# Optimization experiments

Measured on AMD Instinct MI355X. Metric: run time of the kernel, lower is better.

The kernel has to match this reference:

```python
import jax, jax.numpy as jnp
import numpy as np

LONG, LAT, T, B, H, NL = 64, 64, 12, 1024, 256, 2
N = LONG * LAT        # 4096 grid nodes
D = 16 * 16           # 256, lin1_size**2


def _build_adj():
    # Faithful reconstruction of GNNLayer's sparse COO adjacency (duplicates sum,
    # as torch sparse matmul does): identity + symmetric 8-neighbor stencil for
    # interior indices i in [lat+1, (long-1)*lat-1). Each undirected edge is
    # inserted twice (once from each endpoint's loop), so interior weights are 2.
    A = np.zeros((N, N), np.float32)
    A[np.arange(N), np.arange(N)] = 1.0
    i = np.arange(LAT + 1, (LONG - 1) * LAT - 1)
    offs = np.array([-1, 1, LAT, -LAT, LAT - 1, LAT + 1, -LAT - 1, -LAT + 1])
    rows = np.repeat(i, 8)
    cols = (i[:, None] + offs).ravel()
    np.add.at(A, (rows, cols), 1.0)
    np.add.at(A, (cols, rows), 1.0)
    return jnp.asarray(A)


def setup_inputs() -> dict:
    key = jax.random.key(0)
    ks = jax.random.split(key, 12)
    s = lambda k, shape, fan: (jax.random.normal(k, shape, jnp.float32) / np.sqrt(fan)).astype(jnp.float32)
    return {
        "x":  jax.random.normal(ks[0], (T, B, LONG, LAT), jnp.float32),
        "h0": jax.random.normal(ks[1], (NL, B, H), jnp.float32),
        "A":  _build_adj(),
        "W_gnn": s(ks[2], (D, N), N), "b_gnn": jnp.zeros((D,), jnp.float32),
        "W_lin": s(ks[3], (D, D), D), "b_lin": jnp.zeros((D,), jnp.float32),
        "Wih0": s(ks[4], (3 * H, D), D), "Whh0": s(ks[5], (3 * H, H), H),
        "bih0": jnp.zeros((3 * H,), jnp.float32), "bhh0": jnp.zeros((3 * H,), jnp.float32),
        "Wih1": s(ks[6], (3 * H, H), H), "Whh1": s(ks[7], (3 * H, H), H),
        "bih1": jnp.zeros((3 * H,), jnp.float32), "bhh1": jnp.zeros((3 * H,), jnp.float32),
        "Wf0": s(ks[8], (16, H), H), "bf0": jnp.zeros((16,), jnp.float32),
        "Wf1": s(ks[9], (16, 16), 16), "bf1": jnp.zeros((16,), jnp.float32),
        "Wf2": s(ks[10], (1, 16), 16), "bf2": jnp.zeros((1,), jnp.float32),
    }


def _gru_layer(xs, h0, Wih, Whh, bih, bhh):
    # xs: [T, B, In]; PyTorch GRU cell equations, input projection hoisted out of scan.
    xW = jnp.einsum('tbd,hd->tbh', xs, Wih) + bih  # [T, B, 3H]
    def step(h, xw):
        hW = h @ Whh.T + bhh
        ri, zi, ni = jnp.split(xw, 3, axis=-1)
        rh, zh, nh = jnp.split(hW, 3, axis=-1)
        r = jax.nn.sigmoid(ri + rh)
        z = jax.nn.sigmoid(zi + zh)
        n = jnp.tanh(ni + r * nh)
        hn = (1.0 - z) * n + z * h
        return hn, hn
    _, hs = jax.lax.scan(step, h0, xW)
    return hs  # [T, B, H]


def reference(x, h0, A, W_gnn, b_gnn, W_lin, b_lin,
              Wih0, Whh0, bih0, bhh0, Wih1, Whh1, bih1, bhh1,
              Wf0, bf0, Wf1, bf1, Wf2, bf2):
    xf = x.reshape(T, B, N)                                   # flatten grid per step
    h1 = jnp.einsum('tbn,mn->tbm', xf, A)                     # (A @ x^T)^T, all steps at once
    t2 = jax.nn.sigmoid(h1 @ W_gnn.T + b_gnn)                 # GNNLayer lin1 + sigmoid
    t4 = jax.nn.sigmoid(t2 @ W_lin.T + b_lin)                 # HailNet lin1 + sigmoid -> [T,B,256]
    hs = _gru_layer(t4, h0[0], Wih0, Whh0, bih0, bhh0)
    hs = _gru_layer(hs, h0[1], Wih1, Whh1, bih1, bhh1)
    out = hs[-1]                                              # last timestep, [B, H]
    out = jax.nn.sigmoid(out @ Wf0.T + bf0)
    out = jax.nn.sigmoid(out @ Wf1.T + bf1)
    out = jax.nn.sigmoid(out @ Wf2.T + bf2)                   # [B, 1]
    return out
```

## Files before the change

### kernel.cpp

```cpp
#include <hip/hip_runtime.h>
#include <hip/hip_bf16.h>

typedef __bf16 bf16;
typedef __bf16 bf16x4 __attribute__((ext_vector_type(4)));
typedef __bf16 bf16x8 __attribute__((ext_vector_type(8)));
typedef float  f32x4  __attribute__((ext_vector_type(4)));

__device__ __forceinline__ float sigf(float x) { return 1.f / (1.f + __expf(-x)); }
__device__ __forceinline__ float tanhf_fast(float x) { return 1.f - 2.f / (1.f + __expf(2.f * x)); }


__global__ __launch_bounds__(256) void k_weff(const float* __restrict__ A,
                                              const float* __restrict__ Wg,
                                              bf16* __restrict__ Weff) {
    int n = blockIdx.x * 256 + threadIdx.x;
    const int offs[9] = {0, -1, 1, 64, -64, 63, 65, -65, -63};
    float w[9];
    int   m[9];
#pragma unroll
    for (int j = 0; j < 9; j++) {
        int mm = n + offs[j];
        bool ok = (mm >= 0 && mm < 4096);
        m[j] = ok ? mm : 0;
        w[j] = ok ? A[(size_t)n * 4096 + mm] : 0.f;
    }
    int d0 = blockIdx.y * 8;
    for (int d = d0; d < d0 + 8; d++) {
        const float* wr = Wg + (size_t)d * 4096;
        float acc = 0.f;
#pragma unroll
        for (int j = 0; j < 9; j++) acc += w[j] * wr[m[j]];
        Weff[(size_t)d * 4096 + n] = (bf16)acc;
    }
}

__device__ __forceinline__ void prep_conv(const float* __restrict__ a,
                                          bf16* __restrict__ o, int blk) {
    int i = blk * 256 + threadIdx.x;
    o[i] = (bf16)a[i];
}

__device__ __forceinline__ void prep_pack(const float* __restrict__ W,
                                          bf16* __restrict__ out, int blk) {
    int fl = blk * 256 + threadIdx.x;
    int lane = fl & 63;
    int kt = (fl >> 6) & 7;
    int c  = (fl >> 9) % 6;
    int wv = (fl >> 9) / 6;
    int l16 = lane & 15, q = lane >> 4;
    int g = c >> 1;
    int wr = g * 256 + wv * 32 + (c & 1) * 16 + l16;
    const float* p = W + (size_t)wr * 256 + kt * 32 + q * 8;
    float4 f0 = *(const float4*)p, f1 = *(const float4*)(p + 4);
    bf16x8 v;
    v[0] = (bf16)f0.x; v[1] = (bf16)f0.y; v[2] = (bf16)f0.z; v[3] = (bf16)f0.w;
    v[4] = (bf16)f1.x; v[5] = (bf16)f1.y; v[6] = (bf16)f1.z; v[7] = (bf16)f1.w;
    *(bf16x8*)(out + (size_t)fl * 8) = v;
}

__global__ __launch_bounds__(256) void k_prep(const float* __restrict__ Wlin, bf16* __restrict__ WlinB,
                                              const float* __restrict__ Wih0, bf16* __restrict__ Wih0B,
                                              const float* __restrict__ Wih1, bf16* __restrict__ Wih1B,
                                              const float* __restrict__ Whh0, bf16* __restrict__ Wpk0,
                                              const float* __restrict__ Whh1, bf16* __restrict__ Wpk1) {
    int b = blockIdx.x;
    if (b < 256)        prep_conv(Wlin, WlinB, b);
    else if (b < 1024)  prep_conv(Wih0, Wih0B, b - 256);
    else if (b < 1792)  prep_conv(Wih1, Wih1B, b - 1024);
    else if (b < 1888)  prep_pack(Whh0, Wpk0, b - 1792);
    else                prep_pack(Whh1, Wpk1, b - 1888);
}

template <int K, int NTOT, int ACT, bool AF32>
__global__ __launch_bounds__(256) void k_gemm(const void* __restrict__ Ap,
                                              const bf16* __restrict__ Bp,
                                              const float* __restrict__ bias,
                                              void* __restrict__ Cp) {
    __shared__ bf16 sA[64 * 40];
    __shared__ bf16 sB[256 * 40];
    const int tid = threadIdx.x;
    const int lane = tid & 63, wv = tid >> 6;
    const int l16 = lane & 15, q = lane >> 4;
    const int row0 = blockIdx.x * 64;
    const int col0 = blockIdx.y * 256;
    const int ar = tid >> 2, ak = (tid & 3) * 8;

    f32x4 acc[4][4] = {};
    float4 pa0, pa1;
    bf16x8 pab;
    bf16x8 pb[4];

    auto loadA = [&](int k0) {
        if (AF32) {
            const float* p = (const float*)Ap + (size_t)(row0 + ar) * K + k0 + ak;
            pa0 = *(const float4*)p;
            pa1 = *(const float4*)(p + 4);
        } else {
            const bf16* p = (const bf16*)Ap + (size_t)(row0 + ar) * K + k0 + ak;
            pab = *(const bf16x8*)p;
        }
    };
    auto loadB = [&](int k0) {
#pragma unroll
        for (int i = 0; i < 4; i++) {
            int idx = tid + i * 256;
            int r = idx >> 2, kk = (idx & 3) * 8;
            pb[i] = *(const bf16x8*)(Bp + (size_t)(col0 + r) * K + k0 + kk);
        }
    };
    auto stage = [&]() {
        if (AF32) {
            bf16x8 v;
            v[0] = (bf16)pa0.x; v[1] = (bf16)pa0.y; v[2] = (bf16)pa0.z; v[3] = (bf16)pa0.w;
            v[4] = (bf16)pa1.x; v[5] = (bf16)pa1.y; v[6] = (bf16)pa1.z; v[7] = (bf16)pa1.w;
            *(bf16x8*)(sA + ar * 40 + ak) = v;
        } else {
            *(bf16x8*)(sA + ar * 40 + ak) = pab;
        }
#pragma unroll
        for (int i = 0; i < 4; i++) {
            int idx = tid + i * 256;
            int r = idx >> 2, kk = (idx & 3) * 8;
            *(bf16x8*)(sB + r * 40 + kk) = pb[i];
        }
    };

    loadA(0);
    loadB(0);
    const int S = K / 32;
    for (int s = 0; s < S; s++) {
        stage();
        __syncthreads();
        if (s + 1 < S) { loadA((s + 1) * 32); loadB((s + 1) * 32); }
        bf16x8 af[4], bfr[4];
#pragma unroll
        for (int tm = 0; tm < 4; tm++)
            af[tm] = *(bf16x8*)(sA + (tm * 16 + l16) * 40 + q * 8);
#pragma unroll
        for (int tn = 0; tn < 4; tn++)
            bfr[tn] = *(bf16x8*)(sB + (wv * 64 + tn * 16 + l16) * 40 + q * 8);
#pragma unroll
        for (int tm = 0; tm < 4; tm++)
#pragma unroll
            for (int tn = 0; tn < 4; tn++)
                acc[tm][tn] = __builtin_amdgcn_mfma_f32_16x16x32_bf16(
                    af[tm], bfr[tn], acc[tm][tn], 0, 0, 0);
        __syncthreads();
    }

#pragma unroll
    for (int tm = 0; tm < 4; tm++)
#pragma unroll
        for (int tn = 0; tn < 4; tn++)
#pragma unroll
            for (int r = 0; r < 4; r++) {
                int row = row0 + tm * 16 + q * 4 + r;
                int col = col0 + wv * 64 + tn * 16 + l16;
                float v = acc[tm][tn][r] + bias[col];
                if (ACT == 1)
                    ((bf16*)Cp)[(size_t)row * NTOT + col] = (bf16)sigf(v);
                else
                    ((float*)Cp)[(size_t)row * NTOT + col] = v;
            }
}

template <int K, int CHUNK>
__global__ __launch_bounds__(256) void k_gemm_sk(const float* __restrict__ Ap,
                                                 const bf16* __restrict__ Bp,
                                                 float* __restrict__ Cpart) {
    __shared__ bf16 sA[64 * 40];
    __shared__ bf16 sB[256 * 40];
    const int tid = threadIdx.x;
    const int lane = tid & 63, wv = tid >> 6;
    const int l16 = lane & 15, q = lane >> 4;
    const int row0 = blockIdx.x * 64;
    const int kb = blockIdx.y * CHUNK;
    float* Cp = Cpart + (size_t)blockIdx.y * 12288 * 256;
    const int ar = tid >> 2, ak = (tid & 3) * 8;

    f32x4 acc[4][4] = {};
    float4 pa0, pa1;
    bf16x8 pb[4];

    auto loadA = [&](int k0) {
        const float* p = Ap + (size_t)(row0 + ar) * K + kb + k0 + ak;
        pa0 = *(const float4*)p;
        pa1 = *(const float4*)(p + 4);
    };
    auto loadB = [&](int k0) {
#pragma unroll
        for (int i = 0; i < 4; i++) {
            int idx = tid + i * 256;
            int r = idx >> 2, kk = (idx & 3) * 8;
            pb[i] = *(const bf16x8*)(Bp + (size_t)r * K + kb + k0 + kk);
        }
    };
    auto stage = [&]() {
        bf16x8 v;
        v[0] = (bf16)pa0.x; v[1] = (bf16)pa0.y; v[2] = (bf16)pa0.z; v[3] = (bf16)pa0.w;
        v[4] = (bf16)pa1.x; v[5] = (bf16)pa1.y; v[6] = (bf16)pa1.z; v[7] = (bf16)pa1.w;
        *(bf16x8*)(sA + ar * 40 + ak) = v;
#pragma unroll
        for (int i = 0; i < 4; i++) {
            int idx = tid + i * 256;
            int r = idx >> 2, kk = (idx & 3) * 8;
            *(bf16x8*)(sB + r * 40 + kk) = pb[i];
        }
    };

    loadA(0);
    loadB(0);
    const int S = CHUNK / 32;
    for (int s = 0; s < S; s++) {
        stage();
        __syncthreads();
        if (s + 1 < S) { loadA((s + 1) * 32); loadB((s + 1) * 32); }
        bf16x8 af[4], bfr[4];
#pragma unroll
        for (int tm = 0; tm < 4; tm++)
            af[tm] = *(bf16x8*)(sA + (tm * 16 + l16) * 40 + q * 8);
#pragma unroll
        for (int tn = 0; tn < 4; tn++)
            bfr[tn] = *(bf16x8*)(sB + (wv * 64 + tn * 16 + l16) * 40 + q * 8);
#pragma unroll
        for (int tm = 0; tm < 4; tm++)
#pragma unroll
            for (int tn = 0; tn < 4; tn++)
                acc[tm][tn] = __builtin_amdgcn_mfma_f32_16x16x32_bf16(
                    af[tm], bfr[tn], acc[tm][tn], 0, 0, 0);
        __syncthreads();
    }

#pragma unroll
    for (int tm = 0; tm < 4; tm++)
#pragma unroll
        for (int tn = 0; tn < 4; tn++)
#pragma unroll
            for (int r = 0; r < 4; r++) {
                int row = row0 + tm * 16 + q * 4 + r;
                int col = wv * 64 + tn * 16 + l16;
                Cp[(size_t)row * 256 + col] = acc[tm][tn][r];
            }
}

template <int KS>
__global__ __launch_bounds__(256) void k_reduce(const float* __restrict__ Cpart,
                                                const float* __restrict__ bias,
                                                bf16* __restrict__ t2) {
    const size_t STRIDE = (size_t)12288 * 256;
    size_t i = ((size_t)blockIdx.x * 256 + threadIdx.x) * 4;
    f32x4 s = *(const f32x4*)(Cpart + i);
#pragma unroll
    for (int ks = 1; ks < KS; ks++) {
        f32x4 p = *(const f32x4*)(Cpart + ks * STRIDE + i);
        s[0] += p[0]; s[1] += p[1]; s[2] += p[2]; s[3] += p[3];
    }
    int col = (int)(i & 255);
    const float4 b = *(const float4*)(bias + col);
    bf16x4 o;
    o[0] = (bf16)sigf(s[0] + b.x);
    o[1] = (bf16)sigf(s[1] + b.y);
    o[2] = (bf16)sigf(s[2] + b.z);
    o[3] = (bf16)sigf(s[3] + b.w);
    *(bf16x4*)(t2 + i) = o;
}

__global__ __launch_bounds__(512, 2) void k_gru(const float* __restrict__ xw,
                                                const bf16* __restrict__ Wpk,
                                                const float* __restrict__ bhh,
                                                const float* __restrict__ h0,
                                                bf16* __restrict__ hs_out,
                                                float* __restrict__ hfin) {
    __shared__ bf16 hl[16 * 264];
    __shared__ float xwl[16 * 772];
    const int tid = threadIdx.x, lane = tid & 63, wv = tid >> 6;
    const int l16 = lane & 15, q = lane >> 4;
    const int row0 = blockIdx.x * 16;
    const bf16* wb = Wpk + (size_t)wv * 6 * 8 * 64 * 8;

    float bh[6];
#pragma unroll
    for (int c = 0; c < 6; c++) {
        int g = c >> 1;
        bh[c] = bhh[g * 256 + wv * 32 + (c & 1) * 16 + l16];
    }
    float hreg[2][4];
#pragma unroll
    for (int hc = 0; hc < 2; hc++)
#pragma unroll
        for (int r = 0; r < 4; r++) {
            int row = q * 4 + r, col = wv * 32 + hc * 16 + l16;
            float h = h0[(size_t)(row0 + row) * 256 + col];
            hreg[hc][r] = h;
            hl[row * 264 + col] = (bf16)h;
        }
    __syncthreads();

    for (int t = 0; t < 12; t++) {
        {
            const float* gbase = xw + ((size_t)t * 1024 + row0) * 768;
#pragma unroll
            for (int rr = 0; rr < 2; rr++) {
                int row = wv * 2 + rr;
#pragma unroll
                for (int i = 0; i < 3; i++) {
                    const float* gp = gbase + (size_t)row * 768 + i * 256 + lane * 4;
                    float* lp = xwl + row * 772 + i * 256;
                    __builtin_amdgcn_global_load_lds(
                        (const __attribute__((address_space(1))) void*)gp,
                        (__attribute__((address_space(3))) void*)lp,
                        16, 0, 0);
                }
            }
        }
        f32x4 acc[6] = {};
        bf16x8 bc[6], bn[6];
#pragma unroll
        for (int c = 0; c < 6; c++)
            bc[c] = *(const bf16x8*)(wb + ((size_t)(c * 8 + 0) * 64 + lane) * 8);
#pragma unroll
        for (int kt = 0; kt < 8; kt++) {
            bf16x8 a = *(bf16x8*)(hl + l16 * 264 + kt * 32 + q * 8);
            if (kt < 7) {
#pragma unroll
                for (int c = 0; c < 6; c++)
                    bn[c] = *(const bf16x8*)(wb + ((size_t)(c * 8 + kt + 1) * 64 + lane) * 8);
            }
#pragma unroll
            for (int c = 0; c < 6; c++)
                acc[c] = __builtin_amdgcn_mfma_f32_16x16x32_bf16(a, bc[c], acc[c], 0, 0, 0);
#pragma unroll
            for (int c = 0; c < 6; c++) bc[c] = bn[c];
        }
        __syncthreads();
#pragma unroll
        for (int hc = 0; hc < 2; hc++)
#pragma unroll
            for (int r = 0; r < 4; r++) {
                int row = q * 4 + r, col = wv * 32 + hc * 16 + l16;
                const float* xb = xwl + row * 772 + col;
                float rv = sigf(xb[0] + acc[hc][r] + bh[hc]);
                float zv = sigf(xb[256] + acc[2 + hc][r] + bh[2 + hc]);
                float nv = tanhf_fast(xb[512] + rv * (acc[4 + hc][r] + bh[4 + hc]));
                float hn = (1.f - zv) * nv + zv * hreg[hc][r];
                hreg[hc][r] = hn;
                bf16 hb = (bf16)hn;
                hl[row * 264 + col] = hb;
                if (hs_out) hs_out[((size_t)t * 1024 + row0 + row) * 256 + col] = hb;
            }
        __syncthreads();
    }
    if (hfin) {
#pragma unroll
        for (int hc = 0; hc < 2; hc++)
#pragma unroll
            for (int r = 0; r < 4; r++) {
                int row = q * 4 + r, col = wv * 32 + hc * 16 + l16;
                hfin[(size_t)(row0 + row) * 256 + col] = hreg[hc][r];
            }
    }
}

__global__ __launch_bounds__(256) void k_final(const float* __restrict__ h,
                                               const float* __restrict__ Wf0, const float* __restrict__ bf0,
                                               const float* __restrict__ Wf1, const float* __restrict__ bf1,
                                               const float* __restrict__ Wf2, const float* __restrict__ bf2,
                                               float* __restrict__ out) {
    __shared__ float sh[16 * 257];
    __shared__ float sy0[16 * 17];
    __shared__ float sy1[16 * 17];
    int tid = threadIdx.x;
    int r0 = blockIdx.x * 16;
#pragma unroll
    for (int i = 0; i < 16; i++) {
        int idx = tid + i * 256;
        int rr = idx >> 8, cc = idx & 255;
        sh[rr * 257 + cc] = h[(size_t)(r0 + rr) * 256 + cc];
    }
    __syncthreads();
    int rl = tid >> 4, j = tid & 15;
    float acc = bf0[j];
    for (int k = 0; k < 256; k++) acc += sh[rl * 257 + k] * Wf0[j * 256 + k];
    sy0[rl * 17 + j] = sigf(acc);
    __syncthreads();
    float acc1 = bf1[j];
#pragma unroll
    for (int k = 0; k < 16; k++) acc1 += sy0[rl * 17 + k] * Wf1[j * 16 + k];
    sy1[rl * 17 + j] = sigf(acc1);
    __syncthreads();
    if (tid < 16) {
        float a2 = bf2[0];
#pragma unroll
        for (int k = 0; k < 16; k++) a2 += sy1[tid * 17 + k] * Wf2[k];
        out[r0 + tid] = sigf(a2);
    }
}

extern "C" void kernel_launch(void* const* d_in, const int* in_sizes, int n_in,
                              void* d_out, int out_size, void* d_ws, size_t ws_size,
                              hipStream_t stream) {
    const float* x    = (const float*)d_in[0];
    const float* h0   = (const float*)d_in[1];
    const float* A    = (const float*)d_in[2];
    const float* Wgnn = (const float*)d_in[3];
    const float* bgnn = (const float*)d_in[4];
    const float* Wlin = (const float*)d_in[5];
    const float* blin = (const float*)d_in[6];
    const float* Wih0 = (const float*)d_in[7];
    const float* Whh0 = (const float*)d_in[8];
    const float* bih0 = (const float*)d_in[9];
    const float* bhh0 = (const float*)d_in[10];
    const float* Wih1 = (const float*)d_in[11];
    const float* Whh1 = (const float*)d_in[12];
    const float* bih1 = (const float*)d_in[13];
    const float* bhh1 = (const float*)d_in[14];
    const float* Wf0  = (const float*)d_in[15];
    const float* bf0  = (const float*)d_in[16];
    const float* Wf1  = (const float*)d_in[17];
    const float* bf1  = (const float*)d_in[18];
    const float* Wf2  = (const float*)d_in[19];
    const float* bf2  = (const float*)d_in[20];
    float* out = (float*)d_out;

    char* w = (char*)d_ws;
    bf16* Weff  = (bf16*)w;  w += (size_t)256 * 4096 * 2;
    bf16* WlinB = (bf16*)w;  w += (size_t)256 * 256 * 2;
    bf16* Wih0B = (bf16*)w;  w += (size_t)768 * 256 * 2;
    bf16* Wih1B = (bf16*)w;  w += (size_t)768 * 256 * 2;
    bf16* Wpk0  = (bf16*)w;  w += (size_t)768 * 256 * 2;
    bf16* Wpk1  = (bf16*)w;  w += (size_t)768 * 256 * 2;
    bf16* t2    = (bf16*)w;  w += (size_t)12288 * 256 * 2;
    bf16* t4    = (bf16*)w;  w += (size_t)12288 * 256 * 2;
    float* Cpart = (float*)w;
    float* xwb  = (float*)w;
    bf16*  hs   = (bf16*)(w + (size_t)12288 * 768 * 4);
    float* hfin = (float*)(w + (size_t)12288 * 768 * 4 + (size_t)12288 * 256 * 2);
    w += (size_t)4 * 12288 * 256 * 4;
    (void)ws_size;

    k_weff<<<dim3(16, 32), 256, 0, stream>>>(A, Wgnn, Weff);
    k_prep<<<dim3(1984), 256, 0, stream>>>(Wlin, WlinB, Wih0, Wih0B, Wih1, Wih1B,
                                           Whh0, Wpk0, Whh1, Wpk1);

    k_gemm_sk<4096, 2048><<<dim3(192, 2), 256, 0, stream>>>(x, Weff, Cpart);
    k_reduce<2><<<dim3(3072), 256, 0, stream>>>(Cpart, bgnn, t2);
    k_gemm<256, 256, 1, false><<<dim3(192, 1), 256, 0, stream>>>(t2, WlinB, blin, t4);
    k_gemm<256, 768, 0, false><<<dim3(192, 3), 256, 0, stream>>>(t4, Wih0B, bih0, xwb);
    k_gru<<<dim3(64), 512, 0, stream>>>(xwb, Wpk0, bhh0, h0, hs, nullptr);
    k_gemm<256, 768, 0, false><<<dim3(192, 3), 256, 0, stream>>>(hs, Wih1B, bih1, xwb);
    k_gru<<<dim3(64), 512, 0, stream>>>(xwb, Wpk1, bhh1, h0 + (size_t)1024 * 256, nullptr, hfin);
    k_final<<<dim3(64), 256, 0, stream>>>(hfin, Wf0, bf0, Wf1, bf1, Wf2, bf2, out);
}
```

Before: 557.2 us.

## Replace split-K GEMM plus reduce with N-tiled full-K GEMM fused with sigmoid

The large x·Weff GEMM (K=4096) used a split-K scheme writing fp32 partials that a separate reduce kernel summed, biased and passed through a sigmoid. It is now one kernel that tiles N into 64-column blocks (grid 192x4) and runs the full K loop with a 64-wide K step, applying bias and sigmoid in the epilogue. This removes the partial-sum round trip through global memory and one launch. In exchange each x row tile is re-read and re-converted once per N block (four times), and each block does less MFMA work per shared-memory stage.

```diff
diff --git a/kernel.cpp b/kernel.cpp
--- a/kernel.cpp
+++ b/kernel.cpp
@@ -71,6 +71,75 @@
     else                prep_pack(Whh1, Wpk1, b - 1888);
 }
 
+__global__ __launch_bounds__(256) void k_gemm_x(const float* __restrict__ Ap,
+                                                const bf16* __restrict__ Bp,
+                                                const float* __restrict__ bias,
+                                                bf16* __restrict__ Cp) {
+    __shared__ bf16 sA[64 * 72];
+    __shared__ bf16 sB[64 * 72];
+    const int tid = threadIdx.x;
+    const int lane = tid & 63, wv = tid >> 6;
+    const int l16 = lane & 15, q = lane >> 4;
+    const int row0 = blockIdx.x * 64;
+    const int col0 = blockIdx.y * 64;
+    const int ar = tid >> 2, ak = (tid & 3) * 16;
+
+    f32x4 acc[4] = {};
+    float4 pa0, pa1, pa2, pa3;
+    bf16x8 pb0, pb1;
+
+    auto loadA = [&](int k0) {
+        const float* p = Ap + (size_t)(row0 + ar) * 4096 + k0 + ak;
+        pa0 = *(const float4*)p;
+        pa1 = *(const float4*)(p + 4);
+        pa2 = *(const float4*)(p + 8);
+        pa3 = *(const float4*)(p + 12);
+    };
+    auto loadB = [&](int k0) {
+        const bf16* p = Bp + (size_t)(col0 + ar) * 4096 + k0 + ak;
+        pb0 = *(const bf16x8*)p;
+        pb1 = *(const bf16x8*)(p + 8);
+    };
+    auto stage = [&]() {
+        bf16x8 v0, v1;
+        v0[0] = (bf16)pa0.x; v0[1] = (bf16)pa0.y; v0[2] = (bf16)pa0.z; v0[3] = (bf16)pa0.w;
+        v0[4] = (bf16)pa1.x; v0[5] = (bf16)pa1.y; v0[6] = (bf16)pa1.z; v0[7] = (bf16)pa1.w;
+        v1[0] = (bf16)pa2.x; v1[1] = (bf16)pa2.y; v1[2] = (bf16)pa2.z; v1[3] = (bf16)pa2.w;
+        v1[4] = (bf16)pa3.x; v1[5] = (bf16)pa3.y; v1[6] = (bf16)pa3.z; v1[7] = (bf16)pa3.w;
+        *(bf16x8*)(sA + ar * 72 + ak) = v0;
+        *(bf16x8*)(sA + ar * 72 + ak + 8) = v1;
+        *(bf16x8*)(sB + ar * 72 + ak) = pb0;
+        *(bf16x8*)(sB + ar * 72 + ak + 8) = pb1;
+    };
+
+    loadA(0);
+    loadB(0);
+    for (int s = 0; s < 64; s++) {
+        stage();
+        __syncthreads();
+        if (s + 1 < 64) { loadA((s + 1) * 64); loadB((s + 1) * 64); }
+#pragma unroll
+        for (int kk = 0; kk < 2; kk++) {
+            bf16x8 a = *(bf16x8*)(sA + (wv * 16 + l16) * 72 + kk * 32 + q * 8);
+#pragma unroll
+            for (int tn = 0; tn < 4; tn++) {
+                bf16x8 b = *(bf16x8*)(sB + (tn * 16 + l16) * 72 + kk * 32 + q * 8);
+                acc[tn] = __builtin_amdgcn_mfma_f32_16x16x32_bf16(a, b, acc[tn], 0, 0, 0);
+            }
+        }
+        __syncthreads();
+    }
+
+#pragma unroll
+    for (int tn = 0; tn < 4; tn++)
+#pragma unroll
+        for (int r = 0; r < 4; r++) {
+            int row = row0 + wv * 16 + q * 4 + r;
+            int col = col0 + tn * 16 + l16;
+            Cp[(size_t)row * 256 + col] = (bf16)sigf(acc[tn][r] + bias[col]);
+        }
+}
+
 template <int K, int NTOT, int ACT, bool AF32>
 __global__ __launch_bounds__(256) void k_gemm(const void* __restrict__ Ap,
                                               const bf16* __restrict__ Bp,
@@ -162,107 +231,6 @@
                 else
                     ((float*)Cp)[(size_t)row * NTOT + col] = v;
             }
-}
-
-template <int K, int CHUNK>
-__global__ __launch_bounds__(256) void k_gemm_sk(const float* __restrict__ Ap,
-                                                 const bf16* __restrict__ Bp,
-                                                 float* __restrict__ Cpart) {
-    __shared__ bf16 sA[64 * 40];
-    __shared__ bf16 sB[256 * 40];
-    const int tid = threadIdx.x;
-    const int lane = tid & 63, wv = tid >> 6;
-    const int l16 = lane & 15, q = lane >> 4;
-    const int row0 = blockIdx.x * 64;
-    const int kb = blockIdx.y * CHUNK;
-    float* Cp = Cpart + (size_t)blockIdx.y * 12288 * 256;
-    const int ar = tid >> 2, ak = (tid & 3) * 8;
-
-    f32x4 acc[4][4] = {};
-    float4 pa0, pa1;
-    bf16x8 pb[4];
-
-    auto loadA = [&](int k0) {
-        const float* p = Ap + (size_t)(row0 + ar) * K + kb + k0 + ak;
-        pa0 = *(const float4*)p;
-        pa1 = *(const float4*)(p + 4);
-    };
-    auto loadB = [&](int k0) {
-#pragma unroll
-        for (int i = 0; i < 4; i++) {
-            int idx = tid + i * 256;
-            int r = idx >> 2, kk = (idx & 3) * 8;
-            pb[i] = *(const bf16x8*)(Bp + (size_t)r * K + kb + k0 + kk);
-        }
-    };
-    auto stage = [&]() {
-        bf16x8 v;
-        v[0] = (bf16)pa0.x; v[1] = (bf16)pa0.y; v[2] = (bf16)pa0.z; v[3] = (bf16)pa0.w;
-        v[4] = (bf16)pa1.x; v[5] = (bf16)pa1.y; v[6] = (bf16)pa1.z; v[7] = (bf16)pa1.w;
-        *(bf16x8*)(sA + ar * 40 + ak) = v;
-#pragma unroll
-        for (int i = 0; i < 4; i++) {
-            int idx = tid + i * 256;
-            int r = idx >> 2, kk = (idx & 3) * 8;
-            *(bf16x8*)(sB + r * 40 + kk) = pb[i];
-        }
-    };
-
-    loadA(0);
-    loadB(0);
-    const int S = CHUNK / 32;
-    for (int s = 0; s < S; s++) {
-        stage();
-        __syncthreads();
-        if (s + 1 < S) { loadA((s + 1) * 32); loadB((s + 1) * 32); }
-        bf16x8 af[4], bfr[4];
-#pragma unroll
-        for (int tm = 0; tm < 4; tm++)
-            af[tm] = *(bf16x8*)(sA + (tm * 16 + l16) * 40 + q * 8);
-#pragma unroll
-        for (int tn = 0; tn < 4; tn++)
-            bfr[tn] = *(bf16x8*)(sB + (wv * 64 + tn * 16 + l16) * 40 + q * 8);
-#pragma unroll
-        for (int tm = 0; tm < 4; tm++)
-#pragma unroll
-            for (int tn = 0; tn < 4; tn++)
-                acc[tm][tn] = __builtin_amdgcn_mfma_f32_16x16x32_bf16(
-                    af[tm], bfr[tn], acc[tm][tn], 0, 0, 0);
-        __syncthreads();
-    }
-
-#pragma unroll
-    for (int tm = 0; tm < 4; tm++)
-#pragma unroll
-        for (int tn = 0; tn < 4; tn++)
-#pragma unroll
-            for (int r = 0; r < 4; r++) {
-                int row = row0 + tm * 16 + q * 4 + r;
-                int col = wv * 64 + tn * 16 + l16;
-                Cp[(size_t)row * 256 + col] = acc[tm][tn][r];
-            }
-}
-
-template <int KS>
-__global__ __launch_bounds__(256) void k_reduce(const float* __restrict__ Cpart,
-                                                const float* __restrict__ bias,
-                                                bf16* __restrict__ t2) {
-    const size_t STRIDE = (size_t)12288 * 256;
-    size_t i = ((size_t)blockIdx.x * 256 + threadIdx.x) * 4;
-    f32x4 s = *(const f32x4*)(Cpart + i);
-#pragma unroll
-    for (int ks = 1; ks < KS; ks++) {
-        f32x4 p = *(const f32x4*)(Cpart + ks * STRIDE + i);
-        s[0] += p[0]; s[1] += p[1]; s[2] += p[2]; s[3] += p[3];
-    }
-    int col = (int)(i & 255);
-    const float4 b = *(const float4*)(bias + col);
-    bf16x4 o;
-    o[0] = (bf16)sigf(s[0] + b.x);
-    o[1] = (bf16)sigf(s[1] + b.y);
-    o[2] = (bf16)sigf(s[2] + b.z);
-    o[3] = (bf16)sigf(s[3] + b.w);
-    *(bf16x4*)(t2 + i) = o;
 }
 
 __global__ __launch_bounds__(512, 2) void k_gru(const float* __restrict__ xw,
@@ -431,7 +399,6 @@
     bf16* Wpk1  = (bf16*)w;  w += (size_t)768 * 256 * 2;
     bf16* t2    = (bf16*)w;  w += (size_t)12288 * 256 * 2;
     bf16* t4    = (bf16*)w;  w += (size_t)12288 * 256 * 2;
-    float* Cpart = (float*)w;
     float* xwb  = (float*)w;
     bf16*  hs   = (bf16*)(w + (size_t)12288 * 768 * 4);
     float* hfin = (float*)(w + (size_t)12288 * 768 * 4 + (size_t)12288 * 256 * 2);
@@ -442,8 +409,7 @@
     k_prep<<<dim3(1984), 256, 0, stream>>>(Wlin, WlinB, Wih0, Wih0B, Wih1, Wih1B,
                                            Whh0, Wpk0, Whh1, Wpk1);
 
-    k_gemm_sk<4096, 2048><<<dim3(192, 2), 256, 0, stream>>>(x, Weff, Cpart);
-    k_reduce<2><<<dim3(3072), 256, 0, stream>>>(Cpart, bgnn, t2);
+    k_gemm_x<<<dim3(192, 4), 256, 0, stream>>>(x, Weff, bgnn, t2);
     k_gemm<256, 256, 1, false><<<dim3(192, 1), 256, 0, stream>>>(t2, WlinB, blin, t4);
     k_gemm<256, 768, 0, false><<<dim3(192, 3), 256, 0, stream>>>(t4, Wih0B, bih0, xwb);
     k_gru<<<dim3(64), 512, 0, stream>>>(xwb, Wpk0, bhh0, h0, hs, nullptr);
```

After: 554.6 us. About the same (-0.5%).
